# Kernel optimization log

Measured on AMD Instinct MI355X. Metric: run time of the kernel, lower is better.

The kernel has to match this reference:

```python
import jax, jax.numpy as jnp
import numpy as np

N = 100000      # nodes
E = 1600000     # edges
NINP = 64       # input node features
NE = 8          # edge attr channels (spectral supports)
NOUT = 24       # nout1 == nout2
NIN = 2 * NOUT  # 48, hidden width after concat
G = 256         # graphs in batch
EPS = 1e-5


def setup_inputs() -> dict:
    key = jax.random.key(0)
    ks = jax.random.split(key, 40)
    def nrm(i, shape, s=1.0):
        return jax.random.normal(ks[i], shape, dtype=jnp.float32) * s
    inp = {}
    inp["x"] = nrm(0, (N, NINP))
    inp["edge_index"] = jax.random.randint(ks[1], (2, E), 0, N)
    inp["edge_attr"] = nrm(2, (E, NE))
    inp["batch"] = jnp.sort(jax.random.randint(ks[3], (N,), 0, G))
    i = 4
    for l, din in ((1, NINP), (2, NIN), (3, NIN)):
        inp[f"W{l}"] = nrm(i, (NE, din, NOUT), 0.1); i += 1   # SpectConv weight [K,in,out]
        inp[f"b{l}"] = jnp.zeros((NOUT,), jnp.float32)         # SpectConv bias
        inp[f"A{l}"] = nrm(i, (din, NOUT), 0.1); i += 1        # fc11 weight
        inp[f"a{l}"] = jnp.zeros((NOUT,), jnp.float32)
        inp[f"B{l}"] = nrm(i, (din, NOUT), 0.1); i += 1        # fc12 weight
        inp[f"c{l}"] = jnp.zeros((NOUT,), jnp.float32)
        inp[f"g{l}"] = jnp.ones((NIN,), jnp.float32)           # BN gamma
        inp[f"be{l}"] = jnp.zeros((NIN,), jnp.float32)         # BN beta
    inp["F1"] = nrm(i, (NIN, 32), 0.1); i += 1
    inp["f1"] = jnp.zeros((32,), jnp.float32)
    inp["F2"] = nrm(i, (32, 1), 0.1); i += 1
    inp["f2"] = jnp.zeros((1,), jnp.float32)
    return inp


def _ml3(x, src, dst, ea, W, b, A, a, Bm, c):
    # SpectConv (selfconn=False): sum_k segment_sum(ea[:,k]*x[src] -> dst) @ W[k] + b
    xs = x[src]                                    # [E, F] gather
    acc = jnp.zeros((x.shape[0], W.shape[2]), x.dtype)
    for k in range(W.shape[0]):                    # small fixed K=NE loop
        h = jax.ops.segment_sum(ea[:, k:k+1] * xs, dst, num_segments=x.shape[0])
        acc = acc + h @ W[k]
    conv = jax.nn.relu(acc + b)
    gate = jax.nn.relu(x @ A + a) * jnp.tanh(x @ Bm + c)
    return jnp.concatenate([conv, gate], axis=1)   # [N, NIN]


def _bn(x, g, b):
    # BatchNorm1d, training mode (biased batch statistics)
    m = x.mean(0)
    v = x.var(0)
    return (x - m) * jax.lax.rsqrt(v + EPS) * g + b


def reference(x, edge_index, edge_attr, batch,
              W1, b1, A1, a1, B1, c1, g1, be1,
              W2, b2, A2, a2, B2, c2, g2, be2,
              W3, b3, A3, a3, B3, c3, g3, be3,
              F1, f1, F2, f2):
    src, dst = edge_index[0], edge_index[1]
    h = _bn(_ml3(x, src, dst, edge_attr, W1, b1, A1, a1, B1, c1), g1, be1)
    h = _bn(_ml3(h, src, dst, edge_attr, W2, b2, A2, a2, B2, c2), g2, be2)
    h = _bn(_ml3(h, src, dst, edge_attr, W3, b3, A3, a3, B3, c3), g3, be3)
    sums = jax.ops.segment_sum(h, batch, num_segments=G)
    cnts = jax.ops.segment_sum(jnp.ones((h.shape[0], 1), h.dtype), batch, num_segments=G)
    pooled = sums / jnp.maximum(cnts, 1.0)         # global_mean_pool
    return jax.nn.relu(pooled @ F1 + f1) @ F2 + f2  # [G, 1]
```

## Files before the change

### kernel.cpp

```cpp
#include <hip/hip_runtime.h>
#include <hip/hip_fp16.h>
#include <math.h>

#define N_NODES 100000
#define N_EDGES 1600000
#define NGRAPH  256
#define YCOLS   240
#define EPS     1e-5f
#define BNCHUNK 200

typedef _Float16 h2v  __attribute__((ext_vector_type(2)));
typedef _Float16 f16x8 __attribute__((ext_vector_type(8)));
typedef float    f32x4 __attribute__((ext_vector_type(4)));

#if defined(__has_builtin)
#if __has_builtin(__builtin_amdgcn_fdot2)
#define HAVE_FDOT2 1
#endif
#endif

__device__ inline float dot8(float4 yraw, float4 eraw, float acc) {
#ifdef HAVE_FDOT2
  union U { float4 f; h2v v[4]; } y, e;
  y.f = yraw; e.f = eraw;
  acc = __builtin_amdgcn_fdot2(y.v[0], e.v[0], acc, false);
  acc = __builtin_amdgcn_fdot2(y.v[1], e.v[1], acc, false);
  acc = __builtin_amdgcn_fdot2(y.v[2], e.v[2], acc, false);
  acc = __builtin_amdgcn_fdot2(y.v[3], e.v[3], acc, false);
#else
  const __half2* yh = reinterpret_cast<const __half2*>(&yraw);
  const __half2* eh = reinterpret_cast<const __half2*>(&eraw);
#pragma unroll
  for (int i = 0; i < 4; i++) {
    float2 a = __half22float2(yh[i]), b = __half22float2(eh[i]);
    acc += a.x * b.x + a.y * b.y;
  }
#endif
  return acc;
}

__global__ void k_count(const int* __restrict__ dst, int* __restrict__ deg) {
  int e = blockIdx.x * blockDim.x + threadIdx.x;
  if (e < N_EDGES) atomicAdd(&deg[dst[e]], 1);
}

__global__ void k_scan1(const int* __restrict__ deg, int* __restrict__ part,
                        int* __restrict__ bsum) {
  __shared__ int lds[256];
  int t = threadIdx.x;
  int base = blockIdx.x * 1024 + t * 4;
  int v[4]; int s = 0;
#pragma unroll
  for (int i = 0; i < 4; i++) { int idx = base + i; v[i] = (idx < N_NODES) ? deg[idx] : 0; s += v[i]; }
  lds[t] = s; __syncthreads();
  for (int off = 1; off < 256; off <<= 1) {
    int x = (t >= off) ? lds[t - off] : 0;
    __syncthreads();
    lds[t] += x;
    __syncthreads();
  }
  int excl = lds[t] - s;
#pragma unroll
  for (int i = 0; i < 4; i++) { int idx = base + i; if (idx < N_NODES) part[idx] = excl; excl += v[i]; }
  if (t == 255) bsum[blockIdx.x] = lds[255];
}

__global__ void k_scan2(int* __restrict__ bsum, int nb) {
  __shared__ int lds[128];
  int t = threadIdx.x;
  int v = (t < nb) ? bsum[t] : 0;
  lds[t] = v; __syncthreads();
  for (int off = 1; off < 128; off <<= 1) {
    int x = (t >= off) ? lds[t - off] : 0;
    __syncthreads();
    lds[t] += x;
    __syncthreads();
  }
  if (t < nb) bsum[t] = lds[t] - v;
}

__global__ void k_scan3(int* __restrict__ rowptr, const int* __restrict__ bsum,
                        int* __restrict__ cursor) {
  int i = blockIdx.x * blockDim.x + threadIdx.x;
  if (i < N_NODES) {
    int v = rowptr[i] + bsum[i >> 10];
    rowptr[i] = v; cursor[i] = v;
  }
  if (i == 0) rowptr[N_NODES] = N_EDGES;
}

__global__ void k_fill(const int* __restrict__ src, const int* __restrict__ dst,
                       const float* __restrict__ ea, int* __restrict__ cursor,
                       int* __restrict__ esrc, __half* __restrict__ ea_csr) {
  int e = blockIdx.x * blockDim.x + threadIdx.x;
  if (e < N_EDGES) {
    int d = dst[e];
    int pos = atomicAdd(&cursor[d], 1);
    esrc[pos] = src[e];
    float4 a = *reinterpret_cast<const float4*>(ea + (size_t)e * 8);
    float4 b = *reinterpret_cast<const float4*>(ea + (size_t)e * 8 + 4);
    union { __half h[8]; float4 f; } u;
    u.h[0] = __float2half(a.x); u.h[1] = __float2half(a.y);
    u.h[2] = __float2half(a.z); u.h[3] = __float2half(a.w);
    u.h[4] = __float2half(b.x); u.h[5] = __float2half(b.y);
    u.h[6] = __float2half(b.z); u.h[7] = __float2half(b.w);
    *reinterpret_cast<float4*>(ea_csr + (size_t)pos * 8) = u.f;
  }
}

__global__ void k_ghist(const int* __restrict__ batch, int* __restrict__ gcnt) {
  __shared__ int lh[NGRAPH];
  int t = threadIdx.x;
  lh[t] = 0; __syncthreads();
  for (int i = blockIdx.x * 256 + t; i < N_NODES; i += gridDim.x * 256)
    atomicAdd(&lh[batch[i]], 1);
  __syncthreads();
  if (lh[t]) atomicAdd(&gcnt[t], lh[t]);
}

__global__ void k_gscan(const int* __restrict__ gcnt, int* __restrict__ gstart) {
  __shared__ int lds[NGRAPH];
  int t = threadIdx.x;
  int v = gcnt[t]; lds[t] = v; __syncthreads();
  for (int off = 1; off < NGRAPH; off <<= 1) {
    int x = (t >= off) ? lds[t - off] : 0;
    __syncthreads();
    lds[t] += x;
    __syncthreads();
  }
  gstart[t] = lds[t] - v;
  if (t == NGRAPH - 1) gstart[NGRAPH] = lds[NGRAPH - 1];
}

__global__ void k_wcat_h(const float* __restrict__ W, const float* __restrict__ A,
                         const float* __restrict__ B, __half* __restrict__ out,
                         int din) {
  int i = blockIdx.x * blockDim.x + threadIdx.x;
  if (i >= YCOLS * 64) return;
  int p = i / 64, f = i % 64;
  float v = 0.f;
  if (f < din) {
    if (p < 192) { int o = p >> 3, k8 = p & 7; v = W[(k8 * din + f) * 24 + o]; }
    else {
      int q = p - 192, o = q >> 1;
      v = (q & 1) ? B[f * 24 + o] : A[f * 24 + o];
    }
  }
  out[i] = __float2half(v);
}

template <int F>
__global__ __launch_bounds__(256) void k_mm(const float* __restrict__ X,
                                            const __half* __restrict__ Wct,
                                            const float* __restrict__ ss,
                                            const float* __restrict__ ba,
                                            const float* __restrict__ bc,
                                            __half* __restrict__ Yh,
                                            float* __restrict__ h) {
  __shared__ _Float16 sx[64][64];
  int t = threadIdx.x;
  int r0 = blockIdx.x * 64;
  constexpr int F4 = F / 4;
  for (int i = t; i < 64 * F4; i += 256) {
    int row = i / F4, c4 = i - row * F4;
    int grow = r0 + row;
    float4 v = make_float4(0.f, 0.f, 0.f, 0.f);
    if (grow < N_NODES) {
      v = *reinterpret_cast<const float4*>(X + (size_t)grow * F + c4 * 4);
      if (ss) {
        int f = c4 * 4;
        v.x = v.x * ss[f + 0] + ss[48 + f + 0];
        v.y = v.y * ss[f + 1] + ss[48 + f + 1];
        v.z = v.z * ss[f + 2] + ss[48 + f + 2];
        v.w = v.w * ss[f + 3] + ss[48 + f + 3];
      }
    }
    int c = c4 * 4;
    sx[row][c + 0] = (_Float16)v.x;
    sx[row][c + 1] = (_Float16)v.y;
    sx[row][c + 2] = (_Float16)v.z;
    sx[row][c + 3] = (_Float16)v.w;
  }
  if (F == 48) {
    for (int i = t; i < 64 * 16; i += 256) {
      int row = i / 16, k = 48 + (i % 16);
      sx[row][k] = (_Float16)0.f;
    }
  }
  __syncthreads();

  int w = t >> 6, l = t & 63;
  int lo = l & 15;
  int lk = (l >> 4) * 8;
  int g  = l >> 4;
  const f16x8 xb0 = *reinterpret_cast<const f16x8*>(&sx[w * 16 + lo][lk]);
  const f16x8 xb1 = *reinterpret_cast<const f16x8*>(&sx[w * 16 + lo][lk + 32]);
  const _Float16* wct = reinterpret_cast<const _Float16*>(Wct);
  int xg = r0 + w * 16 + lo;

#pragma unroll
  for (int tt = 0; tt < 15; tt++) {
    const f16x8 a0 = *reinterpret_cast<const f16x8*>(wct + (tt * 16 + lo) * 64 + lk);
    const f16x8 a1 = *reinterpret_cast<const f16x8*>(wct + (tt * 16 + lo) * 64 + lk + 32);
    f32x4 acc = {0.f, 0.f, 0.f, 0.f};
    acc = __builtin_amdgcn_mfma_f32_16x16x32_f16(a0, xb0, acc, 0, 0, 0);
    acc = __builtin_amdgcn_mfma_f32_16x16x32_f16(a1, xb1, acc, 0, 0, 0);
    if (xg < N_NODES) {
      if (tt < 12) {
        union { __half h4[4]; uint2 u; } pk;
        pk.h4[0] = __float2half(acc[0]);
        pk.h4[1] = __float2half(acc[1]);
        pk.h4[2] = __float2half(acc[2]);
        pk.h4[3] = __float2half(acc[3]);
        *reinterpret_cast<uint2*>(Yh + (size_t)xg * 192 + tt * 16 + g * 4) = pk.u;
      } else {
        int o0 = (tt - 12) * 8 + g * 2;
        float g0 = fmaxf(acc[0] + ba[o0], 0.f) * tanhf(acc[1] + bc[o0]);
        float g1 = fmaxf(acc[2] + ba[o0 + 1], 0.f) * tanhf(acc[3] + bc[o0 + 1]);
        *reinterpret_cast<float2*>(h + (size_t)xg * 48 + 24 + o0) = make_float2(g0, g1);
      }
    }
  }
}

__global__ __launch_bounds__(192) void k_agg(
    const __half* __restrict__ Yh, const int* __restrict__ rowptr,
    const int* __restrict__ esrc, const __half* __restrict__ ea_csr,
    const float* __restrict__ bconv, float* __restrict__ h) {
  __shared__ float lacc[2][4][24];
  int t = threadIdx.x;
  int ln   = t / 96;
  int slot = (t / 24) % 4;
  int o    = t % 24;
  int n = blockIdx.x * 2 + ln;
  float acc = 0.f;
  if (n < N_NODES) {
    int r0 = rowptr[n], r1 = rowptr[n + 1];
    int idx = r0 + slot;
    for (; idx + 12 < r1; idx += 16) {
      int s0 = esrc[idx], s1 = esrc[idx + 4], s2 = esrc[idx + 8], s3 = esrc[idx + 12];
      float4 e0 = *reinterpret_cast<const float4*>(ea_csr + (size_t)idx * 8);
      float4 e1 = *reinterpret_cast<const float4*>(ea_csr + (size_t)(idx + 4) * 8);
      float4 e2 = *reinterpret_cast<const float4*>(ea_csr + (size_t)(idx + 8) * 8);
      float4 e3 = *reinterpret_cast<const float4*>(ea_csr + (size_t)(idx + 12) * 8);
      float4 y0 = *reinterpret_cast<const float4*>(Yh + (size_t)s0 * 192 + o * 8);
      float4 y1 = *reinterpret_cast<const float4*>(Yh + (size_t)s1 * 192 + o * 8);
      float4 y2 = *reinterpret_cast<const float4*>(Yh + (size_t)s2 * 192 + o * 8);
      float4 y3 = *reinterpret_cast<const float4*>(Yh + (size_t)s3 * 192 + o * 8);
      acc = dot8(y0, e0, acc);
      acc = dot8(y1, e1, acc);
      acc = dot8(y2, e2, acc);
      acc = dot8(y3, e3, acc);
    }
    for (; idx < r1; idx += 4) {
      int s0 = esrc[idx];
      float4 e0 = *reinterpret_cast<const float4*>(ea_csr + (size_t)idx * 8);
      float4 y0 = *reinterpret_cast<const float4*>(Yh + (size_t)s0 * 192 + o * 8);
      acc = dot8(y0, e0, acc);
    }
  }
  lacc[ln][slot][o] = acc;
  __syncthreads();
  if (t < 48) {
    int ln2 = t / 24, oo = t % 24;
    int n2 = blockIdx.x * 2 + ln2;
    if (n2 < N_NODES) {
      float a = lacc[ln2][0][oo] + lacc[ln2][1][oo] + lacc[ln2][2][oo] + lacc[ln2][3][oo];
      h[(size_t)n2 * 48 + oo] = fmaxf(a + bconv[oo], 0.f);
    }
  }
}

__global__ __launch_bounds__(192) void k_bnred1(const float* __restrict__ h,
                                                float* __restrict__ out) {
  __shared__ float lsum[192], lsq[192];
  int t = threadIdx.x;
  int rp = t / 48, c = t % 48;
  int r0 = blockIdx.x * BNCHUNK;
  int r1 = r0 + BNCHUNK; if (r1 > N_NODES) r1 = N_NODES;
  float s = 0.f, q = 0.f;
  for (int r = r0 + rp; r < r1; r += 4) {
    float v = h[(size_t)r * 48 + c];
    s += v; q += v * v;
  }
  lsum[t] = s; lsq[t] = q; __syncthreads();
  if (t < 48) {
    float S = lsum[t] + lsum[t + 48] + lsum[t + 96] + lsum[t + 144];
    float Q = lsq[t] + lsq[t + 48] + lsq[t + 96] + lsq[t + 144];
    out[(size_t)blockIdx.x * 96 + t] = S;
    out[(size_t)blockIdx.x * 96 + 48 + t] = Q;
  }
}

__global__ void k_bnstats(const float* __restrict__ partial, int nblk,
                          const float* __restrict__ g, const float* __restrict__ be,
                          float* __restrict__ ss) {
  __shared__ float ls[256], lq[256];
  int c = blockIdx.x, t = threadIdx.x;
  float s = 0.f, q = 0.f;
  for (int i = t; i < nblk; i += 256) { s += partial[(size_t)i * 96 + c]; q += partial[(size_t)i * 96 + 48 + c]; }
  ls[t] = s; lq[t] = q; __syncthreads();
  for (int off = 128; off > 0; off >>= 1) {
    if (t < off) { ls[t] += ls[t + off]; lq[t] += lq[t + off]; }
    __syncthreads();
  }
  if (t == 0) {
    float mean = ls[0] / (float)N_NODES;
    float var = lq[0] / (float)N_NODES - mean * mean;
    var = fmaxf(var, 0.f);
    float sc = g[c] * rsqrtf(var + EPS);
    ss[c] = sc;
    ss[48 + c] = be[c] - mean * sc;
  }
}

__global__ __launch_bounds__(240) void k_pool2(const float* __restrict__ h,
                                               const int* __restrict__ gstart,
                                               const float* __restrict__ ss,
                                               float* __restrict__ pooled) {
  __shared__ float acc[240];
  int g = blockIdx.x, t = threadIdx.x;
  int o = t % 48, r = t / 48;
  int n0 = gstart[g], n1 = gstart[g + 1];
  float s = 0.f;
  for (int n = n0 + r; n < n1; n += 5) s += h[(size_t)n * 48 + o];
  acc[t] = s; __syncthreads();
  if (t < 48) {
    float tot = acc[t] + acc[t + 48] + acc[t + 96] + acc[t + 144] + acc[t + 192];
    float cnt = (float)(n1 - n0);
    float mean = tot / fmaxf(cnt, 1.f);
    pooled[g * 48 + t] = mean * ss[t] + ss[48 + t];
  }
}

__global__ __launch_bounds__(64) void k_mlp(const float* __restrict__ pooled,
                                            const float* __restrict__ F1,
                                            const float* __restrict__ f1,
                                            const float* __restrict__ F2,
                                            const float* __restrict__ f2,
                                            float* __restrict__ out) {
  __shared__ float p[48];
  int g = blockIdx.x, t = threadIdx.x;
  if (t < 48) p[t] = pooled[g * 48 + t];
  __syncthreads();
  float r = 0.f;
  if (t < 32) {
    float s = f1[t];
#pragma unroll
    for (int c = 0; c < 48; c++) s += p[c] * F1[c * 32 + t];
    r = fmaxf(s, 0.f) * F2[t];
  }
  for (int off = 32; off > 0; off >>= 1) r += __shfl_down(r, off, 64);
  if (t == 0) out[g] = r + f2[0];
}

extern "C" void kernel_launch(void* const* d_in, const int* in_sizes, int n_in,
                              void* d_out, int out_size, void* d_ws, size_t ws_size,
                              hipStream_t stream) {
  const float* x          = (const float*)d_in[0];
  const int*   edge_index = (const int*)d_in[1];
  const float* ea         = (const float*)d_in[2];
  const int*   batch      = (const int*)d_in[3];
  const float *W[3], *bcv[3], *A[3], *ba[3], *B[3], *bc[3], *g[3], *be[3];
  for (int l = 0; l < 3; l++) {
    int base = 4 + l * 8;
    W[l]   = (const float*)d_in[base + 0];
    bcv[l] = (const float*)d_in[base + 1];
    A[l]   = (const float*)d_in[base + 2];
    ba[l]  = (const float*)d_in[base + 3];
    B[l]   = (const float*)d_in[base + 4];
    bc[l]  = (const float*)d_in[base + 5];
    g[l]   = (const float*)d_in[base + 6];
    be[l]  = (const float*)d_in[base + 7];
  }
  const float* F1 = (const float*)d_in[28];
  const float* f1 = (const float*)d_in[29];
  const float* F2 = (const float*)d_in[30];
  const float* f2 = (const float*)d_in[31];
  const int* src = edge_index;
  const int* dst = edge_index + N_EDGES;

  char* w = (char*)d_ws;
  auto alloc = [&](size_t bytes) -> char* {
    char* p = w;
    w += (bytes + 255) & ~(size_t)255;
    return p;
  };
  int nagg = (N_NODES + 1) / 2;
  int nred = (N_NODES + BNCHUNK - 1) / BNCHUNK;

  int*    rowptr  = (int*)alloc((N_NODES + 1) * 4);
  int*    cursor  = (int*)alloc((size_t)N_NODES * 4);
  int*    deg     = (int*)alloc((size_t)N_NODES * 4);
  int*    bsum    = (int*)alloc(128 * 4);
  int*    esrc    = (int*)alloc((size_t)N_EDGES * 4);
  __half* ea_csr  = (__half*)alloc((size_t)N_EDGES * 8 * 2);
  int*    gcnt    = (int*)alloc(NGRAPH * 4);
  int*    gstart  = (int*)alloc((NGRAPH + 1) * 4);
  __half* Wct1    = (__half*)alloc((size_t)YCOLS * 64 * 2);
  __half* Wct2    = (__half*)alloc((size_t)YCOLS * 64 * 2);
  __half* Wct3    = (__half*)alloc((size_t)YCOLS * 64 * 2);
  __half* Yh      = (__half*)alloc((size_t)N_NODES * 192 * 2);
  float*  h0      = (float*)alloc((size_t)N_NODES * 48 * 4);
  float*  h1      = (float*)alloc((size_t)N_NODES * 48 * 4);
  float*  partial2= (float*)alloc((size_t)nred * 96 * 4);
  float*  ss1     = (float*)alloc(96 * 4);
  float*  ss2     = (float*)alloc(96 * 4);
  float*  ss3     = (float*)alloc(96 * 4);
  float*  pooled  = (float*)alloc(NGRAPH * 48 * 4);

  hipMemsetAsync(deg, 0, (size_t)N_NODES * 4, stream);
  hipMemsetAsync(gcnt, 0, NGRAPH * 4, stream);

  k_count<<<(N_EDGES + 255) / 256, 256, 0, stream>>>(dst, deg);
  int nchunk = (N_NODES + 1023) / 1024;
  k_scan1<<<nchunk, 256, 0, stream>>>(deg, rowptr, bsum);
  k_scan2<<<1, 128, 0, stream>>>(bsum, nchunk);
  k_scan3<<<(N_NODES + 255) / 256, 256, 0, stream>>>(rowptr, bsum, cursor);
  k_fill<<<(N_EDGES + 255) / 256, 256, 0, stream>>>(src, dst, ea, cursor, esrc, ea_csr);

  k_ghist<<<64, 256, 0, stream>>>(batch, gcnt);
  k_gscan<<<1, NGRAPH, 0, stream>>>(gcnt, gstart);

  k_wcat_h<<<(YCOLS * 64 + 255) / 256, 256, 0, stream>>>(W[0], A[0], B[0], Wct1, 64);
  k_wcat_h<<<(YCOLS * 64 + 255) / 256, 256, 0, stream>>>(W[1], A[1], B[1], Wct2, 48);
  k_wcat_h<<<(YCOLS * 64 + 255) / 256, 256, 0, stream>>>(W[2], A[2], B[2], Wct3, 48);

  int nmm = (N_NODES + 63) / 64;

  k_mm<64><<<nmm, 256, 0, stream>>>(x, Wct1, nullptr, ba[0], bc[0], Yh, h0);
  k_agg<<<nagg, 192, 0, stream>>>(Yh, rowptr, esrc, ea_csr, bcv[0], h0);
  k_bnred1<<<nred, 192, 0, stream>>>(h0, partial2);
  k_bnstats<<<48, 256, 0, stream>>>(partial2, nred, g[0], be[0], ss1);
  k_mm<48><<<nmm, 256, 0, stream>>>(h0, Wct2, ss1, ba[1], bc[1], Yh, h1);
  k_agg<<<nagg, 192, 0, stream>>>(Yh, rowptr, esrc, ea_csr, bcv[1], h1);
  k_bnred1<<<nred, 192, 0, stream>>>(h1, partial2);
  k_bnstats<<<48, 256, 0, stream>>>(partial2, nred, g[1], be[1], ss2);
  k_mm<48><<<nmm, 256, 0, stream>>>(h1, Wct3, ss2, ba[2], bc[2], Yh, h0);
  k_agg<<<nagg, 192, 0, stream>>>(Yh, rowptr, esrc, ea_csr, bcv[2], h0);
  k_bnred1<<<nred, 192, 0, stream>>>(h0, partial2);
  k_bnstats<<<48, 256, 0, stream>>>(partial2, nred, g[2], be[2], ss3);

  k_pool2<<<NGRAPH, 240, 0, stream>>>(h0, gstart, ss3, pooled);
  k_mlp<<<NGRAPH, 64, 0, stream>>>(pooled, F1, f1, F2, f2, (float*)d_out);
}
```

Before: 637.5 us.

## Fuse BN stats into consumers, merge pool+MLP and weight prep, batch fill

BatchNorm partial sums are now accumulated with global atomics straight into a raw sum buffer. Each consumer kernel derives the scale and shift itself, which removes the separate per-layer stats kernel. Pooling and the final MLP are merged into one kernel, and the three weight-packing launches become one. The CSR fill kernel now handles four edges per thread with batched atomics and nontemporal stores. Together these cut kernel launches and serialization gaps, at the cost of float atomic ordering nondeterminism and an extra memset.

Result: slower. 687.6 us (+7.9%).

```diff
diff --git a/kernel.cpp b/kernel.cpp
--- a/kernel.cpp
+++ b/kernel.cpp
@@ -12,6 +12,7 @@
 typedef _Float16 h2v  __attribute__((ext_vector_type(2)));
 typedef _Float16 f16x8 __attribute__((ext_vector_type(8)));
 typedef float    f32x4 __attribute__((ext_vector_type(4)));
+typedef float    f4v   __attribute__((ext_vector_type(4)));
 
 #if defined(__has_builtin)
 #if __has_builtin(__builtin_amdgcn_fdot2)
@@ -92,19 +93,31 @@
 __global__ void k_fill(const int* __restrict__ src, const int* __restrict__ dst,
                        const float* __restrict__ ea, int* __restrict__ cursor,
                        int* __restrict__ esrc, __half* __restrict__ ea_csr) {
-  int e = blockIdx.x * blockDim.x + threadIdx.x;
-  if (e < N_EDGES) {
-    int d = dst[e];
-    int pos = atomicAdd(&cursor[d], 1);
-    esrc[pos] = src[e];
-    float4 a = *reinterpret_cast<const float4*>(ea + (size_t)e * 8);
-    float4 b = *reinterpret_cast<const float4*>(ea + (size_t)e * 8 + 4);
-    union { __half h[8]; float4 f; } u;
-    u.h[0] = __float2half(a.x); u.h[1] = __float2half(a.y);
-    u.h[2] = __float2half(a.z); u.h[3] = __float2half(a.w);
-    u.h[4] = __float2half(b.x); u.h[5] = __float2half(b.y);
-    u.h[6] = __float2half(b.z); u.h[7] = __float2half(b.w);
-    *reinterpret_cast<float4*>(ea_csr + (size_t)pos * 8) = u.f;
+  const int T = N_EDGES / 4;
+  int tid = blockIdx.x * blockDim.x + threadIdx.x;
+  if (tid >= T) return;
+  int d[4], s[4];
+  float4 a[4], b[4];
+#pragma unroll
+  for (int i = 0; i < 4; i++) {
+    int e = tid + i * T;
+    d[i] = dst[e];
+    s[i] = src[e];
+    a[i] = *reinterpret_cast<const float4*>(ea + (size_t)e * 8);
+    b[i] = *reinterpret_cast<const float4*>(ea + (size_t)e * 8 + 4);
+  }
+  int pos[4];
+#pragma unroll
+  for (int i = 0; i < 4; i++) pos[i] = atomicAdd(&cursor[d[i]], 1);
+#pragma unroll
+  for (int i = 0; i < 4; i++) {
+    __builtin_nontemporal_store(s[i], &esrc[pos[i]]);
+    union { __half h[8]; f4v f; } u;
+    u.h[0] = __float2half(a[i].x); u.h[1] = __float2half(a[i].y);
+    u.h[2] = __float2half(a[i].z); u.h[3] = __float2half(a[i].w);
+    u.h[4] = __float2half(b[i].x); u.h[5] = __float2half(b[i].y);
+    u.h[6] = __float2half(b[i].z); u.h[7] = __float2half(b[i].w);
+    __builtin_nontemporal_store(u.f, reinterpret_cast<f4v*>(ea_csr + (size_t)pos[i] * 8));
   }
 }
 
@@ -132,12 +145,19 @@
   if (t == NGRAPH - 1) gstart[NGRAPH] = lds[NGRAPH - 1];
 }
 
-__global__ void k_wcat_h(const float* __restrict__ W, const float* __restrict__ A,
-                         const float* __restrict__ B, __half* __restrict__ out,
-                         int din) {
+__global__ void k_wcat3(const float* __restrict__ W1, const float* __restrict__ A1,
+                        const float* __restrict__ B1, const float* __restrict__ W2,
+                        const float* __restrict__ A2, const float* __restrict__ B2,
+                        const float* __restrict__ W3, const float* __restrict__ A3,
+                        const float* __restrict__ B3, __half* __restrict__ out) {
   int i = blockIdx.x * blockDim.x + threadIdx.x;
-  if (i >= YCOLS * 64) return;
-  int p = i / 64, f = i % 64;
+  if (i >= 3 * YCOLS * 64) return;
+  int L = i / (YCOLS * 64), r = i - L * (YCOLS * 64);
+  const float *W, *A, *B; int din;
+  if (L == 0)      { W = W1; A = A1; B = B1; din = 64; }
+  else if (L == 1) { W = W2; A = A2; B = B2; din = 48; }
+  else             { W = W3; A = A3; B = B3; din = 48; }
+  int p = r / 64, f = r % 64;
   float v = 0.f;
   if (f < din) {
     if (p < 192) { int o = p >> 3, k8 = p & 7; v = W[(k8 * din + f) * 24 + o]; }
@@ -152,14 +172,25 @@
 template <int F>
 __global__ __launch_bounds__(256) void k_mm(const float* __restrict__ X,
                                             const __half* __restrict__ Wct,
-                                            const float* __restrict__ ss,
+                                            const float* __restrict__ ssraw,
+                                            const float* __restrict__ gg,
+                                            const float* __restrict__ bb,
                                             const float* __restrict__ ba,
                                             const float* __restrict__ bc,
                                             __half* __restrict__ Yh,
                                             float* __restrict__ h) {
   __shared__ _Float16 sx[64][64];
+  __shared__ float ssl[96];
   int t = threadIdx.x;
   int r0 = blockIdx.x * 64;
+  if (ssraw != nullptr && t < 48) {
+    float inv = 1.f / (float)N_NODES;
+    float mean = ssraw[t] * inv;
+    float var = fmaxf(ssraw[48 + t] * inv - mean * mean, 0.f);
+    float sc = gg[t] * rsqrtf(var + EPS);
+    ssl[t] = sc; ssl[48 + t] = bb[t] - mean * sc;
+  }
+  __syncthreads();
   constexpr int F4 = F / 4;
   for (int i = t; i < 64 * F4; i += 256) {
     int row = i / F4, c4 = i - row * F4;
@@ -167,12 +198,12 @@
     float4 v = make_float4(0.f, 0.f, 0.f, 0.f);
     if (grow < N_NODES) {
       v = *reinterpret_cast<const float4*>(X + (size_t)grow * F + c4 * 4);
-      if (ss) {
+      if (ssraw) {
         int f = c4 * 4;
-        v.x = v.x * ss[f + 0] + ss[48 + f + 0];
-        v.y = v.y * ss[f + 1] + ss[48 + f + 1];
-        v.z = v.z * ss[f + 2] + ss[48 + f + 2];
-        v.w = v.w * ss[f + 3] + ss[48 + f + 3];
+        v.x = v.x * ssl[f + 0] + ssl[48 + f + 0];
+        v.y = v.y * ssl[f + 1] + ssl[48 + f + 1];
+        v.z = v.z * ssl[f + 2] + ssl[48 + f + 2];
+        v.w = v.w * ssl[f + 3] + ssl[48 + f + 3];
       }
     }
     int c = c4 * 4;
@@ -271,8 +302,8 @@
   }
 }
 
-__global__ __launch_bounds__(192) void k_bnred1(const float* __restrict__ h,
-                                                float* __restrict__ out) {
+__global__ __launch_bounds__(192) void k_bnred(const float* __restrict__ h,
+                                               float* __restrict__ ssraw) {
   __shared__ float lsum[192], lsq[192];
   int t = threadIdx.x;
   int rp = t / 48, c = t % 48;
@@ -287,39 +318,28 @@
   if (t < 48) {
     float S = lsum[t] + lsum[t + 48] + lsum[t + 96] + lsum[t + 144];
     float Q = lsq[t] + lsq[t + 48] + lsq[t + 96] + lsq[t + 144];
-    out[(size_t)blockIdx.x * 96 + t] = S;
-    out[(size_t)blockIdx.x * 96 + 48 + t] = Q;
-  }
-}
-
-__global__ void k_bnstats(const float* __restrict__ partial, int nblk,
-                          const float* __restrict__ g, const float* __restrict__ be,
-                          float* __restrict__ ss) {
-  __shared__ float ls[256], lq[256];
-  int c = blockIdx.x, t = threadIdx.x;
-  float s = 0.f, q = 0.f;
-  for (int i = t; i < nblk; i += 256) { s += partial[(size_t)i * 96 + c]; q += partial[(size_t)i * 96 + 48 + c]; }
-  ls[t] = s; lq[t] = q; __syncthreads();
-  for (int off = 128; off > 0; off >>= 1) {
-    if (t < off) { ls[t] += ls[t + off]; lq[t] += lq[t + off]; }
-    __syncthreads();
-  }
-  if (t == 0) {
-    float mean = ls[0] / (float)N_NODES;
-    float var = lq[0] / (float)N_NODES - mean * mean;
-    var = fmaxf(var, 0.f);
-    float sc = g[c] * rsqrtf(var + EPS);
-    ss[c] = sc;
-    ss[48 + c] = be[c] - mean * sc;
-  }
-}
-
-__global__ __launch_bounds__(240) void k_pool2(const float* __restrict__ h,
-                                               const int* __restrict__ gstart,
-                                               const float* __restrict__ ss,
-                                               float* __restrict__ pooled) {
+    atomicAdd(&ssraw[t], S);
+    atomicAdd(&ssraw[48 + t], Q);
+  }
+}
+
+__global__ __launch_bounds__(240) void k_poolmlp(
+    const float* __restrict__ h, const int* __restrict__ gstart,
+    const float* __restrict__ ssraw, const float* __restrict__ gg,
+    const float* __restrict__ bb, const float* __restrict__ F1,
+    const float* __restrict__ f1, const float* __restrict__ F2,
+    const float* __restrict__ f2, float* __restrict__ out) {
   __shared__ float acc[240];
+  __shared__ float ssl[96];
+  __shared__ float p[48];
   int g = blockIdx.x, t = threadIdx.x;
+  if (t < 48) {
+    float inv = 1.f / (float)N_NODES;
+    float mean = ssraw[t] * inv;
+    float var = fmaxf(ssraw[48 + t] * inv - mean * mean, 0.f);
+    float sc = gg[t] * rsqrtf(var + EPS);
+    ssl[t] = sc; ssl[48 + t] = bb[t] - mean * sc;
+  }
   int o = t % 48, r = t / 48;
   int n0 = gstart[g], n1 = gstart[g + 1];
   float s = 0.f;
@@ -327,31 +347,21 @@
   acc[t] = s; __syncthreads();
   if (t < 48) {
     float tot = acc[t] + acc[t + 48] + acc[t + 96] + acc[t + 144] + acc[t + 192];
-    float cnt = (float)(n1 - n0);
-    float mean = tot / fmaxf(cnt, 1.f);
-    pooled[g * 48 + t] = mean * ss[t] + ss[48 + t];
-  }
-}
-
-__global__ __launch_bounds__(64) void k_mlp(const float* __restrict__ pooled,
-                                            const float* __restrict__ F1,
-                                            const float* __restrict__ f1,
-                                            const float* __restrict__ F2,
-                                            const float* __restrict__ f2,
-                                            float* __restrict__ out) {
-  __shared__ float p[48];
-  int g = blockIdx.x, t = threadIdx.x;
-  if (t < 48) p[t] = pooled[g * 48 + t];
+    float mean = tot / fmaxf((float)(n1 - n0), 1.f);
+    p[t] = mean * ssl[t] + ssl[48 + t];
+  }
   __syncthreads();
-  float r = 0.f;
-  if (t < 32) {
-    float s = f1[t];
-#pragma unroll
-    for (int c = 0; c < 48; c++) s += p[c] * F1[c * 32 + t];
-    r = fmaxf(s, 0.f) * F2[t];
-  }
-  for (int off = 32; off > 0; off >>= 1) r += __shfl_down(r, off, 64);
-  if (t == 0) out[g] = r + f2[0];
+  if (t < 64) {
+    float rr = 0.f;
+    if (t < 32) {
+      float sum = f1[t];
+#pragma unroll
+      for (int c = 0; c < 48; c++) sum += p[c] * F1[c * 32 + t];
+      rr = fmaxf(sum, 0.f) * F2[t];
+    }
+    for (int off = 32; off > 0; off >>= 1) rr += __shfl_down(rr, off, 64);
+    if (t == 0) out[g] = rr + f2[0];
+  }
 }
 
 extern "C" void kernel_launch(void* const* d_in, const int* in_sizes, int n_in,
@@ -397,50 +407,47 @@
   __half* ea_csr  = (__half*)alloc((size_t)N_EDGES * 8 * 2);
   int*    gcnt    = (int*)alloc(NGRAPH * 4);
   int*    gstart  = (int*)alloc((NGRAPH + 1) * 4);
-  __half* Wct1    = (__half*)alloc((size_t)YCOLS * 64 * 2);
-  __half* Wct2    = (__half*)alloc((size_t)YCOLS * 64 * 2);
-  __half* Wct3    = (__half*)alloc((size_t)YCOLS * 64 * 2);
+  __half* Wct     = (__half*)alloc((size_t)3 * YCOLS * 64 * 2);
+  __half* Wct1    = Wct;
+  __half* Wct2    = Wct + YCOLS * 64;
+  __half* Wct3    = Wct + 2 * YCOLS * 64;
   __half* Yh      = (__half*)alloc((size_t)N_NODES * 192 * 2);
   float*  h0      = (float*)alloc((size_t)N_NODES * 48 * 4);
   float*  h1      = (float*)alloc((size_t)N_NODES * 48 * 4);
-  float*  partial2= (float*)alloc((size_t)nred * 96 * 4);
-  float*  ss1     = (float*)alloc(96 * 4);
-  float*  ss2     = (float*)alloc(96 * 4);
-  float*  ss3     = (float*)alloc(96 * 4);
-  float*  pooled  = (float*)alloc(NGRAPH * 48 * 4);
+  float*  ssraw   = (float*)alloc(3 * 96 * 4);
+  float*  ssraw1  = ssraw;
+  float*  ssraw2  = ssraw + 96;
+  float*  ssraw3  = ssraw + 192;
 
   hipMemsetAsync(deg, 0, (size_t)N_NODES * 4, stream);
   hipMemsetAsync(gcnt, 0, NGRAPH * 4, stream);
+  hipMemsetAsync(ssraw, 0, 3 * 96 * 4, stream);
 
   k_count<<<(N_EDGES + 255) / 256, 256, 0, stream>>>(dst, deg);
   int nchunk = (N_NODES + 1023) / 1024;
   k_scan1<<<nchunk, 256, 0, stream>>>(deg, rowptr, bsum);
   k_scan2<<<1, 128, 0, stream>>>(bsum, nchunk);
   k_scan3<<<(N_NODES + 255) / 256, 256, 0, stream>>>(rowptr, bsum, cursor);
-  k_fill<<<(N_EDGES + 255) / 256, 256, 0, stream>>>(src, dst, ea, cursor, esrc, ea_csr);
+  k_fill<<<(N_EDGES / 4 + 255) / 256, 256, 0, stream>>>(src, dst, ea, cursor, esrc, ea_csr);
 
   k_ghist<<<64, 256, 0, stream>>>(batch, gcnt);
   k_gscan<<<1, NGRAPH, 0, stream>>>(gcnt, gstart);
 
-  k_wcat_h<<<(YCOLS * 64 + 255) / 256, 256, 0, stream>>>(W[0], A[0], B[0], Wct1, 64);
-  k_wcat_h<<<(YCOLS * 64 + 255) / 256, 256, 0, stream>>>(W[1], A[1], B[1], Wct2, 48);
-  k_wcat_h<<<(YCOLS * 64 + 255) / 256, 256, 0, stream>>>(W[2], A[2], B[2], Wct3, 48);
+  k_wcat3<<<(3 * YCOLS * 64 + 255) / 256, 256, 0, stream>>>(
+      W[0], A[0], B[0], W[1], A[1], B[1], W[2], A[2], B[2], Wct);
 
   int nmm = (N_NODES + 63) / 64;
 
-  k_mm<64><<<nmm, 256, 0, stream>>>(x, Wct1, nullptr, ba[0], bc[0], Yh, h0);
+  k_mm<64><<<nmm, 256, 0, stream>>>(x, Wct1, nullptr, nullptr, nullptr, ba[0], bc[0], Yh, h0);
   k_agg<<<nagg, 192, 0, stream>>>(Yh, rowptr, esrc, ea_csr, bcv[0], h0);
-  k_bnred1<<<nred, 192, 0, stream>>>(h0, partial2);
-  k_bnstats<<<48, 256, 0, stream>>>(partial2, nred, g[0], be[0], ss1);
-  k_mm<48><<<nmm, 256, 0, stream>>>(h0, Wct2, ss1, ba[1], bc[1], Yh, h1);
+  k_bnred<<<nred, 192, 0, stream>>>(h0, ssraw1);
+  k_mm<48><<<nmm, 256, 0, stream>>>(h0, Wct2, ssraw1, g[0], be[0], ba[1], bc[1], Yh, h1);
   k_agg<<<nagg, 192, 0, stream>>>(Yh, rowptr, esrc, ea_csr, bcv[1], h1);
-  k_bnred1<<<nred, 192, 0, stream>>>(h1, partial2);
-  k_bnstats<<<48, 256, 0, stream>>>(partial2, nred, g[1], be[1], ss2);
-  k_mm<48><<<nmm, 256, 0, stream>>>(h1, Wct3, ss2, ba[2], bc[2], Yh, h0);
+  k_bnred<<<nred, 192, 0, stream>>>(h1, ssraw2);
+  k_mm<48><<<nmm, 256, 0, stream>>>(h1, Wct3, ssraw2, g[1], be[1], ba[2], bc[2], Yh, h0);
   k_agg<<<nagg, 192, 0, stream>>>(Yh, rowptr, esrc, ea_csr, bcv[2], h0);
-  k_bnred1<<<nred, 192, 0, stream>>>(h0, partial2);
-  k_bnstats<<<48, 256, 0, stream>>>(partial2, nred, g[2], be[2], ss3);
-
-  k_pool2<<<NGRAPH, 240, 0, stream>>>(h0, gstart, ss3, pooled);
-  k_mlp<<<NGRAPH, 64, 0, stream>>>(pooled, F1, f1, F2, f2, (float*)d_out);
-}
+  k_bnred<<<nred, 192, 0, stream>>>(h0, ssraw3);
+
+  k_poolmlp<<<NGRAPH, 240, 0, stream>>>(h0, gstart, ssraw3, g[2], be[2],
+                                        F1, f1, F2, f2, (float*)d_out);
+}
```
